# Optimization experiments

Measured on AMD Instinct MI355X. Metric: run time of the kernel, lower is better.

Reference implementation:

```python
import jax, jax.numpy as jnp
import numpy as np

N, C, HI, WI = 8, 3, 512, 512   # src_img NCHW (input_img_size)
HO, WO = 2048, 2048             # output canvas (output_img_size[2:])
EPS = 1e-8


def _transform_one(img, coor_row):
    """Replicates: sigmoid box params -> theta -> F.affine_grid -> F.grid_sample
    (bilinear, zeros padding, align_corners=False). Theta has zero off-diagonals,
    so the grid is separable in x/y and the bilinear sample factorizes.
    img: [C, HI, WI]; coor_row: [4]. Returns (sample [C,HO,WO], mask [HO,WO])."""
    x = jax.nn.sigmoid(coor_row[0]) * WO
    y = jax.nn.sigmoid(coor_row[1]) * HO
    w = jax.nn.sigmoid(coor_row[2]) * WO
    h = jax.nn.sigmoid(coor_row[3]) * HO
    a = WO / (w + EPS)
    tx = 2.0 / WO * (WO / 2.0 - x) * a
    b = HO / (h + EPS)
    ty = 2.0 / HO * (HO / 2.0 - y) * b
    # affine_grid base coords (align_corners=False): center-of-pixel normalized
    xs = (2.0 * jnp.arange(WO, dtype=img.dtype) + 1.0) / WO - 1.0
    ys = (2.0 * jnp.arange(HO, dtype=img.dtype) + 1.0) / HO - 1.0
    gx = a * xs + tx          # [WO]
    gy = b * ys + ty          # [HO]
    # grid_sample unnormalize (align_corners=False)
    ix = ((gx + 1.0) * WI - 1.0) / 2.0
    iy = ((gy + 1.0) * HI - 1.0) / 2.0
    x0f = jnp.floor(ix); y0f = jnp.floor(iy)
    wx1 = ix - x0f; wx0 = 1.0 - wx1
    wy1 = iy - y0f; wy0 = 1.0 - wy1
    x0 = x0f.astype(jnp.int32); x1 = x0 + 1
    y0 = y0f.astype(jnp.int32); y1 = y0 + 1
    vx0 = ((x0 >= 0) & (x0 < WI)).astype(img.dtype)
    vx1 = ((x1 >= 0) & (x1 < WI)).astype(img.dtype)
    vy0 = ((y0 >= 0) & (y0 < HI)).astype(img.dtype)
    vy1 = ((y1 >= 0) & (y1 < HI)).astype(img.dtype)
    x0c = jnp.clip(x0, 0, WI - 1); x1c = jnp.clip(x1, 0, WI - 1)
    y0c = jnp.clip(y0, 0, HI - 1); y1c = jnp.clip(y1, 0, HI - 1)
    wyv0 = wy0 * vy0; wyv1 = wy1 * vy1
    wxv0 = wx0 * vx0; wxv1 = wx1 * vx1
    # separable bilinear gather with zero padding
    rows = img[:, y0c, :] * wyv0[None, :, None] + img[:, y1c, :] * wyv1[None, :, None]  # [C,HO,WI]
    samp = rows[:, :, x0c] * wxv0[None, None, :] + rows[:, :, x1c] * wxv1[None, None, :]  # [C,HO,WO]
    # grid_sample of an all-ones mask == sum of in-bounds bilinear weights (separable)
    mask = (wyv0 + wyv1)[:, None] * (wxv0 + wxv1)[None, :]  # [HO,WO]
    return samp, mask


def _composite(src_img, bg_img, coor):
    def step(bg, inp):
        img, c = inp
        s, m = _transform_one(img, c)
        bg = bg * (1.0 - m)[None, None] + (s * m[None])[None]
        return bg, None
    bg, _ = jax.lax.scan(step, bg_img, (src_img, coor))
    return bg


def setup_inputs() -> dict:
    key = jax.random.key(0)
    k1, k2, k3 = jax.random.split(key, 3)
    src_img = jax.random.normal(k1, (N, C, HI, WI), dtype=jnp.float32)
    bg_img = jax.random.uniform(k2, (1, C, HO, WO), dtype=jnp.float32)
    coor = jax.random.normal(k3, (N, 4), dtype=jnp.float32)  # nn.Parameter
    return {"src_img": src_img, "bg_img": bg_img, "coor": coor}


def reference(src_img, bg_img, coor):
    return _composite(src_img, bg_img, coor)
```

## Files before the change

### kernel.cpp

```cpp
#include <hip/hip_runtime.h>

#define WI 512
#define HI 512
#define WO 2048
#define HO 2048
#define NIMG 8
#define CCH 3
#define EPS 1e-8f
#define PLANE (HI * WI)

#define TPB  256
#define SEG  1024
#define PXT  4
#define CAP  520

struct SState {
    float wy0, wy1, my;
    int   t0a, R, lim;
    int   valid;
};

__device__ __forceinline__ SState calc_state(const float4 P, const float ys,
                                             const int wo0) {
    SState st; st.valid = 0; st.wy0 = st.wy1 = st.my = 0.0f;
    st.t0a = 0; st.R = 0; st.lim = 0;
    const float gy  = P.z * ys + P.w;
    const float iy  = ((gy + 1.0f) * (float)HI - 1.0f) * 0.5f;
    const float y0f = floorf(iy);
    const float fy1 = iy - y0f;
    const float fy0 = 1.0f - fy1;
    const float y1f = y0f + 1.0f;
    const float v0  = (y0f >= 0.0f && y0f < (float)HI) ? 1.0f : 0.0f;
    const float v1  = (y1f >= 0.0f && y1f < (float)HI) ? 1.0f : 0.0f;
    st.wy0 = fy0 * v0;
    st.wy1 = fy1 * v1;
    st.my  = st.wy0 + st.wy1;
    if (!(st.my > 0.0f)) return st;

    const float a  = P.x, tx = P.y;
    const float xsf = (2.0f * (float)wo0 + 1.0f) / (float)WO - 1.0f;
    const float xsl = (2.0f * (float)(wo0 + SEG - 1) + 1.0f) / (float)WO - 1.0f;
    const float ixf = ((a * xsf + tx + 1.0f) * (float)WI - 1.0f) * 0.5f;
    const float ixl = ((a * xsl + tx + 1.0f) * (float)WI - 1.0f) * 0.5f;
    if (ixl <= -1.0f || ixf >= (float)WI) return st;

    const int t0 = (int)fminf(fmaxf(floorf(ixf), 0.0f), (float)(WI - 1));
    const int t1 = (int)fminf(fmaxf(floorf(ixl) + 1.0f, 0.0f), (float)(WI - 1));
    st.t0a = t0 & ~3;
    int R = (t1 - st.t0a + 4) & ~3;
    if (R > WI - st.t0a) R = WI - st.t0a;
    st.R   = R;
    st.lim = t1 - st.t0a;
    st.valid = 1;
    return st;
}

__launch_bounds__(TPB)
__global__ void diffcomp_v8(const float* __restrict__ src,
                            const float* __restrict__ bg,
                            const float* __restrict__ coor,
                            float* __restrict__ out) {
    __shared__ float  cs[2][CCH][CAP];
    __shared__ float4 prm[NIMG];

    const int tid = threadIdx.x;
    const int b   = blockIdx.x;
    const int row = b >> 1;
    const int wo0 = (b & 1) << 10;

    if (tid < NIMG) {
        const float cx  = coor[tid * 4 + 0];
        const float cy  = coor[tid * 4 + 1];
        const float cw  = coor[tid * 4 + 2];
        const float chh = coor[tid * 4 + 3];
        const float x = (1.0f / (1.0f + expf(-cx))) * (float)WO;
        const float y = (1.0f / (1.0f + expf(-cy))) * (float)HO;
        const float w = (1.0f / (1.0f + expf(-cw))) * (float)WO;
        const float h = (1.0f / (1.0f + expf(-chh))) * (float)HO;
        const float a  = (float)WO / (w + EPS);
        const float tx = (2.0f / (float)WO) * ((float)WO * 0.5f - x) * a;
        const float bb = (float)HO / (h + EPS);
        const float ty = (2.0f / (float)HO) * ((float)HO * 0.5f - y) * bb;
        prm[tid] = make_float4(a, tx, bb, ty);
    }
    __syncthreads();

    const float ys = (2.0f * (float)row + 1.0f) / (float)HO - 1.0f;

    unsigned cov = 0u;
#pragma unroll
    for (int n = 0; n < NIMG; n++) {
        if (calc_state(prm[n], ys, wo0).valid) cov |= (1u << n);
    }

    float xsv[PXT];
#pragma unroll
    for (int p = 0; p < PXT; p++) {
        const int wo = wo0 + p * TPB + tid;
        xsv[p] = (2.0f * (float)wo + 1.0f) / (float)WO - 1.0f;
    }

    const int base = row * WO + wo0 + tid;
    float acc[CCH][PXT];
#pragma unroll
    for (int c = 0; c < CCH; c++)
#pragma unroll
        for (int p = 0; p < PXT; p++)
            acc[c][p] = bg[c * HO * WO + base + p * TPB];

    if (cov) {
        float4 A0[CCH], A1[CCH], B0[CCH], B1[CCH];
        SState stA, stB;

        auto load_img = [&](int n, SState& st, float4* r0, float4* r1) {
            st = calc_state(prm[n], ys, wo0);
            const int xo = tid << 2;
            if (xo < st.R) {
                const float* ib = src + n * (CCH * PLANE) + st.t0a + xo;
                const float gy  = prm[n].z * ys + prm[n].w;
                const float iy  = ((gy + 1.0f) * (float)HI - 1.0f) * 0.5f;
                const float y0f = floorf(iy);
                const int y0o = (int)fminf(fmaxf(y0f, 0.0f), (float)(HI - 1)) * WI;
                const int y1o = (int)fminf(fmaxf(y0f + 1.0f, 0.0f), (float)(HI - 1)) * WI;
#pragma unroll
                for (int c = 0; c < CCH; c++) {
                    r0[c] = *(const float4*)(ib + c * PLANE + y0o);
                    r1[c] = *(const float4*)(ib + c * PLANE + y1o);
                }
            }
        };

        auto commit_img = [&](int slot, const SState& st,
                              const float4* r0, const float4* r1) {
            const int xo = tid << 2;
            if (xo < st.R) {
#pragma unroll
                for (int c = 0; c < CCH; c++) {
                    float4 rc;
                    rc.x = r0[c].x * st.wy0 + r1[c].x * st.wy1;
                    rc.y = r0[c].y * st.wy0 + r1[c].y * st.wy1;
                    rc.z = r0[c].z * st.wy0 + r1[c].z * st.wy1;
                    rc.w = r0[c].w * st.wy0 + r1[c].w * st.wy1;
                    *(float4*)&cs[slot][c][xo] = rc;
                }
            }
        };

        auto blend_img = [&](int slot, int n, const SState& st) {
            const float a  = prm[n].x;
            const float tx = prm[n].y;
#pragma unroll
            for (int p = 0; p < PXT; p++) {
                const float gx  = a * xsv[p] + tx;
                const float ix  = ((gx + 1.0f) * (float)WI - 1.0f) * 0.5f;
                const float x0f = floorf(ix);
                const float fx1 = ix - x0f;
                const float fx0 = 1.0f - fx1;
                const float x1f = x0f + 1.0f;
                const float v0  = (x0f >= 0.0f && x0f < (float)WI) ? 1.0f : 0.0f;
                const float v1  = (x1f >= 0.0f && x1f < (float)WI) ? 1.0f : 0.0f;
                const float wx0 = fx0 * v0;
                const float wx1 = fx1 * v1;
                int x0r = (int)fminf(fmaxf(x0f, 0.0f), (float)(WI - 1)) - st.t0a;
                int x1r = (int)fminf(fmaxf(x1f, 0.0f), (float)(WI - 1)) - st.t0a;
                x0r = min(max(x0r, 0), st.lim);
                x1r = min(max(x1r, 0), st.lim);
                const float m  = st.my * (wx0 + wx1);
                const float om = 1.0f - m;
#pragma unroll
                for (int c = 0; c < CCH; c++) {
                    const float q0 = cs[slot][c][x0r];
                    const float q1 = cs[slot][c][x1r];
                    const float sc = q0 * wx0 + q1 * wx1;
                    acc[c][p] = acc[c][p] * om + sc * m;
                }
            }
        };

        int cur = (int)__builtin_ctz(cov);
        unsigned rest = cov & (cov - 1u);

        load_img(cur, stA, A0, A1);
        int s = 0;
        while (true) {
            const int nxt = rest ? (int)__builtin_ctz(rest) : -1;
            if (nxt >= 0) load_img(nxt, stB, B0, B1);
            commit_img(s, stA, A0, A1);
            __syncthreads();
            blend_img(s, cur, stA);
            if (nxt < 0) break;
            cur = nxt;
            rest &= rest - 1u;
            stA = stB;
#pragma unroll
            for (int c = 0; c < CCH; c++) { A0[c] = B0[c]; A1[c] = B1[c]; }
            s ^= 1;
        }
    }

#pragma unroll
    for (int c = 0; c < CCH; c++)
#pragma unroll
        for (int p = 0; p < PXT; p++)
            out[c * HO * WO + base + p * TPB] = acc[c][p];
}

extern "C" void kernel_launch(void* const* d_in, const int* in_sizes, int n_in,
                              void* d_out, int out_size, void* d_ws, size_t ws_size,
                              hipStream_t stream) {
    const float* src  = (const float*)d_in[0];
    const float* bg   = (const float*)d_in[1];
    const float* coor = (const float*)d_in[2];
    float* out = (float*)d_out;
    (void)d_ws; (void)ws_size;

    hipLaunchKernelGGL(diffcomp_v8, dim3(HO * (WO / SEG)), dim3(TPB), 0, stream,
                       src, bg, coor, out);
}
```

Baseline: 134.3 us.

## Precompute per-column x sampling table and permute block order

Adds a small pre-kernel that computes, for each image and output column, the horizontal bilinear weights and clamped source indices, storing them as int4 in the workspace. The main kernel reads these from the table instead of recomputing floor and clamp math per pixel. It also fetches an adjacent pair of shared-memory values and selects between them. Blocks are visited in a scrambled order (multiply by 1031 mod 4096) to balance load across rows with differing image coverage. The cost is an extra launch and a table read per pixel per image; a fallback path is kept for when the workspace is too small.

```diff
diff --git a/kernel.cpp b/kernel.cpp
--- a/kernel.cpp
+++ b/kernel.cpp
@@ -16,14 +16,14 @@
 
 struct SState {
     float wy0, wy1, my;
-    int   t0a, R, lim;
+    int   t0a, R, brmax;
     int   valid;
 };
 
 __device__ __forceinline__ SState calc_state(const float4 P, const float ys,
                                              const int wo0) {
     SState st; st.valid = 0; st.wy0 = st.wy1 = st.my = 0.0f;
-    st.t0a = 0; st.R = 0; st.lim = 0;
+    st.t0a = 0; st.R = 0; st.brmax = 0;
     const float gy  = P.z * ys + P.w;
     const float iy  = ((gy + 1.0f) * (float)HI - 1.0f) * 0.5f;
     const float y0f = floorf(iy);
@@ -49,24 +49,56 @@
     st.t0a = t0 & ~3;
     int R = (t1 - st.t0a + 4) & ~3;
     if (R > WI - st.t0a) R = WI - st.t0a;
-    st.R   = R;
-    st.lim = t1 - st.t0a;
+    st.R     = R;
+    const int lim = t1 - st.t0a;
+    st.brmax = (lim > 1) ? (lim - 1) : 0;
     st.valid = 1;
     return st;
 }
 
+__global__ void diffcomp_xtab(const float* __restrict__ coor,
+                              int4* __restrict__ xtab) {
+    const int idx = blockIdx.x * 256 + threadIdx.x;
+    const int n   = idx >> 11;
+    const int wo  = idx & 2047;
+
+    const float cx = coor[n * 4 + 0];
+    const float cw = coor[n * 4 + 2];
+    const float x = (1.0f / (1.0f + expf(-cx))) * (float)WO;
+    const float w = (1.0f / (1.0f + expf(-cw))) * (float)WO;
+    const float a  = (float)WO / (w + EPS);
+    const float tx = (2.0f / (float)WO) * ((float)WO * 0.5f - x) * a;
+
+    const float xs  = (2.0f * (float)wo + 1.0f) / (float)WO - 1.0f;
+    const float gx  = a * xs + tx;
+    const float ix  = ((gx + 1.0f) * (float)WI - 1.0f) * 0.5f;
+    const float x0f = floorf(ix);
+    const float fx1 = ix - x0f;
+    const float fx0 = 1.0f - fx1;
+    const float x1f = x0f + 1.0f;
+    const float v0  = (x0f >= 0.0f && x0f < (float)WI) ? 1.0f : 0.0f;
+    const float v1  = (x1f >= 0.0f && x1f < (float)WI) ? 1.0f : 0.0f;
+    int4 e;
+    e.x = __float_as_int(fx0 * v0);
+    e.y = __float_as_int(fx1 * v1);
+    e.z = (int)fminf(fmaxf(x0f, 0.0f), (float)(WI - 1));
+    e.w = (int)fminf(fmaxf(x1f, 0.0f), (float)(WI - 1));
+    xtab[idx] = e;
+}
+
 __launch_bounds__(TPB)
-__global__ void diffcomp_v8(const float* __restrict__ src,
+__global__ void diffcomp_v9(const float* __restrict__ src,
                             const float* __restrict__ bg,
                             const float* __restrict__ coor,
+                            const int4* __restrict__ xtab,
                             float* __restrict__ out) {
     __shared__ float  cs[2][CCH][CAP];
     __shared__ float4 prm[NIMG];
 
     const int tid = threadIdx.x;
-    const int b   = blockIdx.x;
-    const int row = b >> 1;
-    const int wo0 = (b & 1) << 10;
+    const int bs  = (int)((blockIdx.x * 1031u) & 4095u);
+    const int row = bs >> 1;
+    const int wo0 = (bs & 1) << 10;
 
     if (tid < NIMG) {
         const float cx  = coor[tid * 4 + 0];
@@ -93,6 +125,144 @@
         if (calc_state(prm[n], ys, wo0).valid) cov |= (1u << n);
     }
 
+    const int base = row * WO + wo0 + tid;
+    float acc[CCH][PXT];
+#pragma unroll
+    for (int c = 0; c < CCH; c++)
+#pragma unroll
+        for (int p = 0; p < PXT; p++)
+            acc[c][p] = bg[c * HO * WO + base + p * TPB];
+
+    if (cov) {
+        float4 A0[CCH], A1[CCH], B0[CCH], B1[CCH];
+        SState stA, stB;
+
+        auto load_img = [&](int n, SState& st, float4* r0, float4* r1) {
+            st = calc_state(prm[n], ys, wo0);
+            const int xo = tid << 2;
+            if (xo < st.R) {
+                const float* ib = src + n * (CCH * PLANE) + st.t0a + xo;
+                const float gy  = prm[n].z * ys + prm[n].w;
+                const float iy  = ((gy + 1.0f) * (float)HI - 1.0f) * 0.5f;
+                const float y0f = floorf(iy);
+                const int y0o = (int)fminf(fmaxf(y0f, 0.0f), (float)(HI - 1)) * WI;
+                const int y1o = (int)fminf(fmaxf(y0f + 1.0f, 0.0f), (float)(HI - 1)) * WI;
+#pragma unroll
+                for (int c = 0; c < CCH; c++) {
+                    r0[c] = *(const float4*)(ib + c * PLANE + y0o);
+                    r1[c] = *(const float4*)(ib + c * PLANE + y1o);
+                }
+            }
+        };
+
+        auto commit_img = [&](int slot, const SState& st,
+                              const float4* r0, const float4* r1) {
+            const int xo = tid << 2;
+            if (xo < st.R) {
+#pragma unroll
+                for (int c = 0; c < CCH; c++) {
+                    float4 rc;
+                    rc.x = r0[c].x * st.wy0 + r1[c].x * st.wy1;
+                    rc.y = r0[c].y * st.wy0 + r1[c].y * st.wy1;
+                    rc.z = r0[c].z * st.wy0 + r1[c].z * st.wy1;
+                    rc.w = r0[c].w * st.wy0 + r1[c].w * st.wy1;
+                    *(float4*)&cs[slot][c][xo] = rc;
+                }
+            }
+        };
+
+        auto blend_img = [&](int slot, int n, const SState& st) {
+            const int4* xt = xtab + (n << 11) + wo0 + tid;
+#pragma unroll
+            for (int p = 0; p < PXT; p++) {
+                const int4 e = xt[p * TPB];
+                const float wx0 = __int_as_float(e.x);
+                const float wx1 = __int_as_float(e.y);
+                const int x0r = e.z - st.t0a;
+                const int x1r = e.w - st.t0a;
+                const int br  = min(x0r, st.brmax);
+                const bool hi0 = x0r > br;
+                const bool hi1 = x1r > br;
+                const float m  = st.my * (wx0 + wx1);
+                const float om = 1.0f - m;
+#pragma unroll
+                for (int c = 0; c < CCH; c++) {
+                    const float qa = cs[slot][c][br];
+                    const float qb = cs[slot][c][br + 1];
+                    const float q0 = hi0 ? qb : qa;
+                    const float q1 = hi1 ? qb : qa;
+                    const float sc = q0 * wx0 + q1 * wx1;
+                    acc[c][p] = acc[c][p] * om + sc * m;
+                }
+            }
+        };
+
+        int cur = (int)__builtin_ctz(cov);
+        unsigned rest = cov & (cov - 1u);
+
+        load_img(cur, stA, A0, A1);
+        int s = 0;
+        while (true) {
+            const int nxt = rest ? (int)__builtin_ctz(rest) : -1;
+            if (nxt >= 0) load_img(nxt, stB, B0, B1);
+            commit_img(s, stA, A0, A1);
+            __syncthreads();
+            blend_img(s, cur, stA);
+            if (nxt < 0) break;
+            cur = nxt;
+            rest &= rest - 1u;
+            stA = stB;
+#pragma unroll
+            for (int c = 0; c < CCH; c++) { A0[c] = B0[c]; A1[c] = B1[c]; }
+            s ^= 1;
+        }
+    }
+
+#pragma unroll
+    for (int c = 0; c < CCH; c++)
+#pragma unroll
+        for (int p = 0; p < PXT; p++)
+            out[c * HO * WO + base + p * TPB] = acc[c][p];
+}
+
+__launch_bounds__(TPB)
+__global__ void diffcomp_v8fb(const float* __restrict__ src,
+                              const float* __restrict__ bg,
+                              const float* __restrict__ coor,
+                              float* __restrict__ out) {
+    __shared__ float  cs[2][CCH][CAP];
+    __shared__ float4 prm[NIMG];
+
+    const int tid = threadIdx.x;
+    const int b   = blockIdx.x;
+    const int row = b >> 1;
+    const int wo0 = (b & 1) << 10;
+
+    if (tid < NIMG) {
+        const float cx  = coor[tid * 4 + 0];
+        const float cy  = coor[tid * 4 + 1];
+        const float cw  = coor[tid * 4 + 2];
+        const float chh = coor[tid * 4 + 3];
+        const float x = (1.0f / (1.0f + expf(-cx))) * (float)WO;
+        const float y = (1.0f / (1.0f + expf(-cy))) * (float)HO;
+        const float w = (1.0f / (1.0f + expf(-cw))) * (float)WO;
+        const float h = (1.0f / (1.0f + expf(-chh))) * (float)HO;
+        const float a  = (float)WO / (w + EPS);
+        const float tx = (2.0f / (float)WO) * ((float)WO * 0.5f - x) * a;
+        const float bb = (float)HO / (h + EPS);
+        const float ty = (2.0f / (float)HO) * ((float)HO * 0.5f - y) * bb;
+        prm[tid] = make_float4(a, tx, bb, ty);
+    }
+    __syncthreads();
+
+    const float ys = (2.0f * (float)row + 1.0f) / (float)HO - 1.0f;
+
+    unsigned cov = 0u;
+#pragma unroll
+    for (int n = 0; n < NIMG; n++) {
+        if (calc_state(prm[n], ys, wo0).valid) cov |= (1u << n);
+    }
+
     float xsv[PXT];
 #pragma unroll
     for (int p = 0; p < PXT; p++) {
@@ -163,8 +333,9 @@
                 const float wx1 = fx1 * v1;
                 int x0r = (int)fminf(fmaxf(x0f, 0.0f), (float)(WI - 1)) - st.t0a;
                 int x1r = (int)fminf(fmaxf(x1f, 0.0f), (float)(WI - 1)) - st.t0a;
-                x0r = min(max(x0r, 0), st.lim);
-                x1r = min(max(x1r, 0), st.lim);
+                const int lim = st.brmax + 1;
+                x0r = min(max(x0r, 0), lim);
+                x1r = min(max(x1r, 0), lim);
                 const float m  = st.my * (wx0 + wx1);
                 const float om = 1.0f - m;
 #pragma unroll
@@ -212,8 +383,17 @@
     const float* bg   = (const float*)d_in[1];
     const float* coor = (const float*)d_in[2];
     float* out = (float*)d_out;
-    (void)d_ws; (void)ws_size;
-
-    hipLaunchKernelGGL(diffcomp_v8, dim3(HO * (WO / SEG)), dim3(TPB), 0, stream,
-                       src, bg, coor, out);
-}
+
+    const size_t xtab_bytes = (size_t)NIMG * 2048 * sizeof(int4);
+
+    if (ws_size >= xtab_bytes) {
+        int4* xtab = (int4*)d_ws;
+        hipLaunchKernelGGL(diffcomp_xtab, dim3(NIMG * 2048 / 256), dim3(256),
+                           0, stream, coor, xtab);
+        hipLaunchKernelGGL(diffcomp_v9, dim3(HO * (WO / SEG)), dim3(TPB),
+                           0, stream, src, bg, coor, xtab, out);
+    } else {
+        hipLaunchKernelGGL(diffcomp_v8fb, dim3(HO * (WO / SEG)), dim3(TPB),
+                           0, stream, src, bg, coor, out);
+    }
+}
```

Measured after the change: 144.6 us. 1.08x slower.
